# Optimization experiments

Measured on AMD Instinct MI355X. Metric: run time of the kernel, lower is better.

Reference implementation:

```python
import jax, jax.numpy as jnp
import numpy as np

N, D, E = 524288, 64, 4  # tokens, feature dim (d_in=64 default), num_expert=4


def setup_inputs() -> dict:
    key = jax.random.key(0)
    ks = jax.random.split(key, 5)
    s = 0.02
    return {
        "x": jax.random.normal(ks[0], (N, D), jnp.float32),
        "w_gate_a": jax.random.normal(ks[1], (D, E), jnp.float32) * s,
        "w_exp_a": jax.random.normal(ks[2], (E, D, D), jnp.float32) * s,
        "b_exp_a": jnp.zeros((E, D), jnp.float32),
        "w_gate_b": jax.random.normal(ks[3], (D, E), jnp.float32) * s,
        "w_exp_b": jax.random.normal(ks[4], (E, D, D), jnp.float32) * s,
        "b_exp_b": jnp.zeros((E, D), jnp.float32),
    }


def _moe_layer(x, w_gate, w_exp, b_exp):
    # Soft MoE: softmax gate over experts, each expert is (x - b_e) @ W_e.
    # Noise and PWLayer dropout are eval-mode identities.
    gates = jax.nn.softmax(x @ w_gate, axis=-1)            # [N, E]
    shifted = x[:, None, :] - b_exp[None, :, :]            # [N, E, D]
    expert_out = jnp.einsum('ned,edf->nef', shifted, w_exp)  # [N, E, D]
    return jnp.einsum('ne,nef->nf', gates, expert_out)     # [N, D]


def reference(x, w_gate_a, w_exp_a, b_exp_a, w_gate_b, w_exp_b, b_exp_b):
    residual = x
    h = _moe_layer(x, w_gate_a, w_exp_a, b_exp_a)
    # self.act is None (default) and nn.Dropout(0.5) is identity in eval mode
    h = _moe_layer(h, w_gate_b, w_exp_b, b_exp_b)
    return h + residual
```

## Files before the change

### kernel.cpp

```cpp
#include <hip/hip_runtime.h>
#include <math.h>


typedef __attribute__((ext_vector_type(8))) short short8;
typedef __attribute__((ext_vector_type(4))) short short4v;
typedef __attribute__((ext_vector_type(4))) float floatx4;

__device__ __forceinline__ float bf2f(unsigned short s) {
    unsigned int u = ((unsigned int)s) << 16;
    return __builtin_bit_cast(float, u);
}
__device__ __forceinline__ short f2bf(float f) {
    unsigned int u = __builtin_bit_cast(unsigned int, f);
    u += 0x7fffu + ((u >> 16) & 1u);
    return (short)(u >> 16);
}

#define NBLOCKS 512
#define TPW 4

__device__ __forceinline__ float ldf(const void* p, int isbf, int idx) {
    return isbf ? bf2f(((const unsigned short*)p)[idx]) : ((const float*)p)[idx];
}

__global__ __launch_bounds__(256, 2)
void moe2_fused(const void* __restrict__ x,
                const void* __restrict__ wg_a,
                const void* __restrict__ we_a,
                const void* __restrict__ be_a,
                const void* __restrict__ wg_b,
                const void* __restrict__ we_b,
                const void* __restrict__ be_b,
                void* __restrict__ outv)
{
    __shared__ alignas(16) short sB[2][17408];
    __shared__ float sC[2][4][64];
    __shared__ alignas(16) short sStage[4][1152];
    __shared__ int sBad[7];

    const int tid = threadIdx.x;

    const void* ps[7] = {x, wg_a, we_a, be_a, wg_b, we_b, be_b};
    if (tid < 7) sBad[tid] = 0;
    __syncthreads();
    if (tid < 64) {
        #pragma unroll
        for (int b = 0; b < 7; ++b) {
            const unsigned short s = ((const unsigned short*)ps[b])[2 * tid];
            const float a = fabsf(bf2f(s));
            const bool sane = (s == 0) || (a >= 9.3e-10f && a <= 1.1e9f);
            if (!sane) atomicAdd(&sBad[b], 1);
        }
    }
    __syncthreads();
    const int fx  = (sBad[0] < 16);
    const int fga = (sBad[1] < 16), fwa = (sBad[2] < 16), fba = (sBad[3] < 16);
    const int fgb = (sBad[4] < 16), fwb = (sBad[5] < 16), fbb = (sBad[6] < 16);

    for (int idx = tid; idx < 2 * 17 * 2 * 64; idx += 256) {
        const int L   = idx / 2176;
        const int rem = idx - L * 2176;
        const int t   = rem >> 7;
        const int kap = (rem >> 6) & 1;
        const int l2  = rem & 63;
        const int kb  = kap * 32 + (l2 >> 4) * 8;
        const int cc  = l2 & 15;
        const void* we = L ? we_b : we_a;
        const void* wg = L ? wg_b : wg_a;
        const int  fwe = L ? fwb : fwa;
        const int  fwg = L ? fgb : fga;
        short* dst = &sB[L][rem * 8];
        if (t < 16) {
            const int e = t >> 2;
            const int f = (t & 3) * 16 + cc;
            #pragma unroll
            for (int j = 0; j < 8; ++j)
                dst[j] = f2bf(ldf(we, fwe, (e * 64 + kb + j) * 64 + f));
        } else {
            #pragma unroll
            for (int j = 0; j < 8; ++j)
                dst[j] = (cc < 4) ? f2bf(ldf(wg, fwg, (kb + j) * 4 + cc)) : (short)0;
        }
    }
    for (int idx = tid; idx < 512; idx += 256) {
        const int L = idx >> 8;
        const int e = (idx >> 6) & 3;
        const int f = idx & 63;
        const void* we = L ? we_b : we_a;
        const void* be = L ? be_b : be_a;
        const int  fwe = L ? fwb : fwa;
        const int  fbe = L ? fbb : fba;
        float s = 0.f;
        for (int d = 0; d < 64; ++d)
            s += ldf(be, fbe, e * 64 + d) * ldf(we, fwe, (e * 64 + d) * 64 + f);
        sC[L][e][f] = s;
    }
    __syncthreads();

    const int l  = tid & 63;
    const int wv = tid >> 6;
    const int c  = l & 15;
    const int q  = l >> 4;
    short* stg = &sStage[wv][0];

    auto runLayer = [&](const short8 (&aF)[4][2], const int L, float (&acc)[4][4][4]) {
        const short* BL = &sB[L][0];
        floatx4 gA[4];
        {
            const short8 B0 = *(const short8*)&BL[(16 * 2 + 0) * 512 + l * 8];
            const short8 B1 = *(const short8*)&BL[(16 * 2 + 1) * 512 + l * 8];
            #pragma unroll
            for (int s = 0; s < 4; ++s) {
                floatx4 z = {0.f, 0.f, 0.f, 0.f};
                z = __builtin_amdgcn_mfma_f32_16x16x32_bf16(aF[s][0], B0, z, 0, 0, 0);
                z = __builtin_amdgcn_mfma_f32_16x16x32_bf16(aF[s][1], B1, z, 0, 0, 0);
                gA[s] = z;
            }
        }
        #pragma unroll
        for (int s = 0; s < 4; ++s) {
            float lg[4][4];
            #pragma unroll
            for (int e = 0; e < 4; ++e)
                #pragma unroll
                for (int r = 0; r < 4; ++r)
                    lg[e][r] = __shfl(gA[s][r], (l & 48) + e, 64);
            short gv[4];
            #pragma unroll
            for (int r = 0; r < 4; ++r) {
                const float m0 = fmaxf(fmaxf(lg[0][r], lg[1][r]), fmaxf(lg[2][r], lg[3][r]));
                const float e0 = __expf(lg[0][r] - m0);
                const float e1 = __expf(lg[1][r] - m0);
                const float e2 = __expf(lg[2][r] - m0);
                const float e3 = __expf(lg[3][r] - m0);
                const float inv = 1.f / (e0 + e1 + e2 + e3);
                const float mine = (c == 0) ? e0 : (c == 1) ? e1 : (c == 2) ? e2 : e3;
                gv[r] = f2bf(mine * inv);
            }
            if (c < 4) {
                short4v pk = {gv[0], gv[1], gv[2], gv[3]};
                *(short4v*)&stg[(s * 4 + c) * 16 + 4 * q] = pk;
            }
        }

        #pragma unroll
        for (int s = 0; s < 4; ++s)
            #pragma unroll
            for (int tt = 0; tt < 4; ++tt)
                #pragma unroll
                for (int r = 0; r < 4; ++r)
                    acc[s][tt][r] = 0.f;

        #pragma unroll
        for (int e = 0; e < 4; ++e) {
            float gse[4][4];
            #pragma unroll
            for (int s = 0; s < 4; ++s) {
                const short4v gp = *(const short4v*)&stg[(s * 4 + e) * 16 + 4 * q];
                #pragma unroll
                for (int r = 0; r < 4; ++r)
                    gse[s][r] = bf2f((unsigned short)gp[r]);
            }
            #pragma unroll
            for (int tt = 0; tt < 4; ++tt) {
                const int t = e * 4 + tt;
                const short8 B0 = *(const short8*)&BL[(t * 2 + 0) * 512 + l * 8];
                const short8 B1 = *(const short8*)&BL[(t * 2 + 1) * 512 + l * 8];
                const float ce = sC[L][e][tt * 16 + c];
                #pragma unroll
                for (int s = 0; s < 4; ++s) {
                    floatx4 z = {0.f, 0.f, 0.f, 0.f};
                    z = __builtin_amdgcn_mfma_f32_16x16x32_bf16(aF[s][0], B0, z, 0, 0, 0);
                    z = __builtin_amdgcn_mfma_f32_16x16x32_bf16(aF[s][1], B1, z, 0, 0, 0);
                    #pragma unroll
                    for (int r = 0; r < 4; ++r)
                        acc[s][tt][r] += gse[s][r] * (z[r] - ce);
                }
            }
        }
    };

    const int waveGlobal = blockIdx.x * 4 + wv;
    for (int it = 0; it < TPW; ++it) {
        const int tile = waveGlobal * TPW + it;
        const size_t tok0 = (size_t)tile * 64;

        short8 xF[4][2];
        if (fx) {
            const unsigned short* xu = (const unsigned short*)x;
            #pragma unroll
            for (int s = 0; s < 4; ++s)
                #pragma unroll
                for (int k = 0; k < 2; ++k)
                    xF[s][k] = *(const short8*)(xu + (tok0 + s * 16 + c) * 64 + k * 32 + q * 8);
        } else {
            const float* xf = (const float*)x;
            #pragma unroll
            for (int s = 0; s < 4; ++s)
                #pragma unroll
                for (int k = 0; k < 2; ++k) {
                    const float* xr = xf + (tok0 + s * 16 + c) * 64 + k * 32 + q * 8;
                    const floatx4 v0 = *(const floatx4*)xr;
                    const floatx4 v1 = *(const floatx4*)(xr + 4);
                    short8 f;
                    #pragma unroll
                    for (int j = 0; j < 4; ++j) { f[j] = f2bf(v0[j]); f[4 + j] = f2bf(v1[j]); }
                    xF[s][k] = f;
                }
        }

        float acc[4][4][4];
        runLayer(xF, 0, acc);

        short8 hF[4][2];
        #pragma unroll
        for (int s = 0; s < 4; ++s) {
            #pragma unroll
            for (int tt = 0; tt < 4; ++tt)
                #pragma unroll
                for (int r = 0; r < 4; ++r)
                    stg[(4 * q + r) * 72 + tt * 16 + c] = f2bf(acc[s][tt][r]);
            hF[s][0] = *(const short8*)&stg[c * 72 + 0 + q * 8];
            hF[s][1] = *(const short8*)&stg[c * 72 + 32 + q * 8];
        }

        runLayer(hF, 1, acc);

        if (fx) {
            unsigned short* ob = (unsigned short*)outv;
            #pragma unroll
            for (int s = 0; s < 4; ++s) {
                #pragma unroll
                for (int tt = 0; tt < 4; ++tt)
                    #pragma unroll
                    for (int r = 0; r < 4; ++r)
                        stg[(4 * q + r) * 72 + tt * 16 + c] = f2bf(acc[s][tt][r]);
                #pragma unroll
                for (int k = 0; k < 2; ++k) {
                    const short8 v = *(const short8*)&stg[c * 72 + k * 32 + q * 8];
                    short8 o;
                    #pragma unroll
                    for (int j = 0; j < 8; ++j)
                        o[j] = f2bf(bf2f((unsigned short)v[j]) + bf2f((unsigned short)xF[s][k][j]));
                    *(short8*)(ob + (tok0 + s * 16 + c) * 64 + k * 32 + q * 8) = o;
                }
            }
        } else {
            const float* xf = (const float*)x;
            float* of = (float*)outv;
            #pragma unroll
            for (int s = 0; s < 4; ++s)
                #pragma unroll
                for (int tt = 0; tt < 4; ++tt)
                    #pragma unroll
                    for (int r = 0; r < 4; ++r) {
                        const size_t o = (tok0 + s * 16 + 4 * q + r) * 64 + tt * 16 + c;
                        of[o] = acc[s][tt][r] + xf[o];
                    }
        }
    }
}

extern "C" void kernel_launch(void* const* d_in, const int* in_sizes, int n_in,
                              void* d_out, int out_size, void* d_ws, size_t ws_size,
                              hipStream_t stream) {
    hipLaunchKernelGGL(moe2_fused, dim3(NBLOCKS), dim3(256), 0, stream,
                       d_in[0], d_in[1], d_in[2], d_in[3], d_in[4], d_in[5], d_in[6],
                       d_out);
}
```

Before: 356.2 us.

## Use butterfly-shuffle softmax, fp32 gates, vector FMA accumulate, and LDS-staged vectorized fp32 output

The gate softmax now uses xor-shuffle butterfly reductions across the 4 expert lanes with a hardware reciprocal, replacing 16 broadcast shuffles per row. Gates are staged in LDS as fp32 instead of bf16, which drops the conversions. Accumulation uses vector FMA on floatx4, and token offsets switch to 32-bit unsigned arithmetic. The fp32 output path is transposed through LDS so the residual read and output write use 128-bit coalesced accesses instead of scattered scalar accesses. The trade-off is more LDS traffic and slightly less precise reciprocal math.

```diff
diff --git a/kernel.cpp b/kernel.cpp
--- a/kernel.cpp
+++ b/kernel.cpp
@@ -14,6 +14,13 @@
     unsigned int u = __builtin_bit_cast(unsigned int, f);
     u += 0x7fffu + ((u >> 16) & 1u);
     return (short)(u >> 16);
+}
+__device__ __forceinline__ float fastrcp(float x) {
+#if __has_builtin(__builtin_amdgcn_rcpf)
+    return __builtin_amdgcn_rcpf(x);
+#else
+    return 1.f / x;
+#endif
 }
 
 #define NBLOCKS 512
@@ -101,9 +108,10 @@
     const int wv = tid >> 6;
     const int c  = l & 15;
     const int q  = l >> 4;
-    short* stg = &sStage[wv][0];
-
-    auto runLayer = [&](const short8 (&aF)[4][2], const int L, float (&acc)[4][4][4]) {
+    short* stg  = &sStage[wv][0];
+    float* gstg = (float*)&sStage[wv][0];
+
+    auto runLayer = [&](const short8 (&aF)[4][2], const int L, floatx4 (&acc)[4][4]) {
         const short* BL = &sB[L][0];
         floatx4 gA[4];
         {
@@ -119,62 +127,45 @@
         }
         #pragma unroll
         for (int s = 0; s < 4; ++s) {
-            float lg[4][4];
-            #pragma unroll
-            for (int e = 0; e < 4; ++e)
-                #pragma unroll
-                for (int r = 0; r < 4; ++r)
-                    lg[e][r] = __shfl(gA[s][r], (l & 48) + e, 64);
-            short gv[4];
+            floatx4 g4;
             #pragma unroll
             for (int r = 0; r < 4; ++r) {
-                const float m0 = fmaxf(fmaxf(lg[0][r], lg[1][r]), fmaxf(lg[2][r], lg[3][r]));
-                const float e0 = __expf(lg[0][r] - m0);
-                const float e1 = __expf(lg[1][r] - m0);
-                const float e2 = __expf(lg[2][r] - m0);
-                const float e3 = __expf(lg[3][r] - m0);
-                const float inv = 1.f / (e0 + e1 + e2 + e3);
-                const float mine = (c == 0) ? e0 : (c == 1) ? e1 : (c == 2) ? e2 : e3;
-                gv[r] = f2bf(mine * inv);
-            }
-            if (c < 4) {
-                short4v pk = {gv[0], gv[1], gv[2], gv[3]};
-                *(short4v*)&stg[(s * 4 + c) * 16 + 4 * q] = pk;
-            }
+                const float v = gA[s][r];
+                float m = fmaxf(v, __shfl_xor(v, 1, 64));
+                m = fmaxf(m, __shfl_xor(m, 2, 64));
+                const float ev = __expf(v - m);
+                float sm = ev + __shfl_xor(ev, 1, 64);
+                sm += __shfl_xor(sm, 2, 64);
+                g4[r] = ev * fastrcp(sm);
+            }
+            if (c < 4) *(floatx4*)&gstg[(s * 4 + c) * 16 + 4 * q] = g4;
         }
 
         #pragma unroll
         for (int s = 0; s < 4; ++s)
             #pragma unroll
             for (int tt = 0; tt < 4; ++tt)
-                #pragma unroll
-                for (int r = 0; r < 4; ++r)
-                    acc[s][tt][r] = 0.f;
+                acc[s][tt] = (floatx4){0.f, 0.f, 0.f, 0.f};
 
         #pragma unroll
         for (int e = 0; e < 4; ++e) {
-            float gse[4][4];
-            #pragma unroll
-            for (int s = 0; s < 4; ++s) {
-                const short4v gp = *(const short4v*)&stg[(s * 4 + e) * 16 + 4 * q];
-                #pragma unroll
-                for (int r = 0; r < 4; ++r)
-                    gse[s][r] = bf2f((unsigned short)gp[r]);
-            }
+            floatx4 ge[4];
+            #pragma unroll
+            for (int s = 0; s < 4; ++s)
+                ge[s] = *(const floatx4*)&gstg[(s * 4 + e) * 16 + 4 * q];
             #pragma unroll
             for (int tt = 0; tt < 4; ++tt) {
                 const int t = e * 4 + tt;
                 const short8 B0 = *(const short8*)&BL[(t * 2 + 0) * 512 + l * 8];
                 const short8 B1 = *(const short8*)&BL[(t * 2 + 1) * 512 + l * 8];
                 const float ce = sC[L][e][tt * 16 + c];
+                const floatx4 cv = {ce, ce, ce, ce};
                 #pragma unroll
                 for (int s = 0; s < 4; ++s) {
                     floatx4 z = {0.f, 0.f, 0.f, 0.f};
                     z = __builtin_amdgcn_mfma_f32_16x16x32_bf16(aF[s][0], B0, z, 0, 0, 0);
                     z = __builtin_amdgcn_mfma_f32_16x16x32_bf16(aF[s][1], B1, z, 0, 0, 0);
-                    #pragma unroll
-                    for (int r = 0; r < 4; ++r)
-                        acc[s][tt][r] += gse[s][r] * (z[r] - ce);
+                    acc[s][tt] = __builtin_elementwise_fma(ge[s], z - cv, acc[s][tt]);
                 }
             }
         }
@@ -183,7 +174,7 @@
     const int waveGlobal = blockIdx.x * 4 + wv;
     for (int it = 0; it < TPW; ++it) {
         const int tile = waveGlobal * TPW + it;
-        const size_t tok0 = (size_t)tile * 64;
+        const unsigned tok0 = (unsigned)tile * 64u;
 
         short8 xF[4][2];
         if (fx) {
@@ -192,14 +183,14 @@
             for (int s = 0; s < 4; ++s)
                 #pragma unroll
                 for (int k = 0; k < 2; ++k)
-                    xF[s][k] = *(const short8*)(xu + (tok0 + s * 16 + c) * 64 + k * 32 + q * 8);
+                    xF[s][k] = *(const short8*)(xu + (tok0 + s * 16 + c) * 64u + k * 32 + q * 8);
         } else {
             const float* xf = (const float*)x;
             #pragma unroll
             for (int s = 0; s < 4; ++s)
                 #pragma unroll
                 for (int k = 0; k < 2; ++k) {
-                    const float* xr = xf + (tok0 + s * 16 + c) * 64 + k * 32 + q * 8;
+                    const float* xr = xf + (tok0 + s * 16 + c) * 64u + k * 32 + q * 8;
                     const floatx4 v0 = *(const floatx4*)xr;
                     const floatx4 v1 = *(const floatx4*)(xr + 4);
                     short8 f;
@@ -209,7 +200,7 @@
                 }
         }
 
-        float acc[4][4][4];
+        floatx4 acc[4][4];
         runLayer(xF, 0, acc);
 
         short8 hF[4][2];
@@ -242,21 +233,31 @@
                     #pragma unroll
                     for (int j = 0; j < 8; ++j)
                         o[j] = f2bf(bf2f((unsigned short)v[j]) + bf2f((unsigned short)xF[s][k][j]));
-                    *(short8*)(ob + (tok0 + s * 16 + c) * 64 + k * 32 + q * 8) = o;
+                    *(short8*)(ob + (tok0 + s * 16 + c) * 64u + k * 32 + q * 8) = o;
                 }
             }
         } else {
             const float* xf = (const float*)x;
             float* of = (float*)outv;
             #pragma unroll
-            for (int s = 0; s < 4; ++s)
-                #pragma unroll
-                for (int tt = 0; tt < 4; ++tt)
-                    #pragma unroll
-                    for (int r = 0; r < 4; ++r) {
-                        const size_t o = (tok0 + s * 16 + 4 * q + r) * 64 + tt * 16 + c;
-                        of[o] = acc[s][tt][r] + xf[o];
-                    }
+            for (int s = 0; s < 4; ++s) {
+                #pragma unroll
+                for (int H = 0; H < 2; ++H) {
+                    #pragma unroll
+                    for (int t2 = 0; t2 < 2; ++t2)
+                        #pragma unroll
+                        for (int r = 0; r < 4; ++r)
+                            gstg[(4 * q + r) * 36 + t2 * 16 + c] = acc[s][H * 2 + t2][r];
+                    const float* srcp = &gstg[c * 36 + q * 8];
+                    const unsigned ro = (tok0 + s * 16 + c) * 64u + H * 32 + q * 8;
+                    const floatx4 v0 = *(const floatx4*)(srcp);
+                    const floatx4 v1 = *(const floatx4*)(srcp + 4);
+                    const floatx4 x0 = *(const floatx4*)(xf + ro);
+                    const floatx4 x1 = *(const floatx4*)(xf + ro + 4);
+                    *(floatx4*)(of + ro)     = v0 + x0;
+                    *(floatx4*)(of + ro + 4) = v1 + x1;
+                }
+            }
         }
     }
 }
```

After: 343.0 us. 1.04x faster.
